# Performance work log

Measured on AMD Instinct MI355X. Metric: run time of the kernel, lower is better.

The kernel has to match this reference:

```python
import jax, jax.numpy as jnp
import numpy as np

B, S, E = 2, 2048, 2048
NH, NKV = 32, 8
HD = E // NH  # 64


def apply_rope(x, cos, sin):
    # x: [B, S, H, D]; cos/sin: [S, D]
    s, d = x.shape[1], x.shape[3]
    c = cos[:s, :d][None, :, None, :]
    sn = sin[:s, :d][None, :, None, :]
    x_rot = jnp.concatenate([-x[..., d // 2:], x[..., : d // 2]], axis=-1)
    return x * c + x_rot * sn


def setup_inputs() -> dict:
    key = jax.random.key(0)
    ks = jax.random.split(key, 6)
    x = jax.random.normal(ks[0], (B, S, E), dtype=jnp.float32)
    mask = jnp.ones((B, S), dtype=bool)
    # RoPE tables [S, HD]
    inv_freq = 1.0 / (10000.0 ** (jnp.arange(0, HD, 2, dtype=jnp.float32) / HD))
    freqs = jnp.arange(S, dtype=jnp.float32)[:, None] * inv_freq[None, :]
    emb = jnp.concatenate([freqs, freqs], axis=-1)  # [S, HD]
    cos = jnp.cos(emb)
    sin = jnp.sin(emb)
    sc = 1.0 / np.sqrt(E)
    Wq = jax.random.normal(ks[1], (E, E), dtype=jnp.float32) * sc
    Wk = jax.random.normal(ks[2], (NKV * HD, E), dtype=jnp.float32) * sc
    Wv = jax.random.normal(ks[3], (NKV * HD, E), dtype=jnp.float32) * sc
    Wo = jax.random.normal(ks[4], (E, E), dtype=jnp.float32) * sc
    return {"x": x, "mask": mask, "cos": cos, "sin": sin,
            "Wq": Wq, "Wk": Wk, "Wv": Wv, "Wo": Wo}


def reference(x, mask, cos, sin, Wq, Wk, Wv, Wo):
    b, s, e = x.shape
    scale = 1.0 / np.sqrt(HD)
    q = (x @ Wq.T).reshape(b, s, NH, HD)
    k = (x @ Wk.T).reshape(b, s, NKV, HD)
    v = (x @ Wv.T).reshape(b, s, NKV, HD)
    q = apply_rope(q, cos, sin)
    k = apply_rope(k, cos, sin)
    rep = NH // NKV
    # expand kv heads: [B,S,NKV,HD] -> [B,S,NH,HD]
    k = jnp.repeat(k, rep, axis=2)
    v = jnp.repeat(v, rep, axis=2)
    # [B,H,S,S]
    scores = jnp.einsum('bqhd,bkhd->bhqk', q, k) * scale
    causal = jnp.tril(jnp.ones((s, s), dtype=bool))
    combined = mask[:, None, None, :] & causal[None, None, :, :]
    scores = jnp.where(combined, scores, -jnp.inf)
    attn = jax.nn.softmax(scores, axis=-1)
    ctx = jnp.einsum('bhqk,bkhd->bqhd', attn, v).reshape(b, s, e)
    return ctx @ Wo.T
```

## Files before the change

### kernel.cpp

```cpp
#include <hip/hip_runtime.h>


typedef __attribute__((ext_vector_type(4))) float f32x4;
typedef __attribute__((ext_vector_type(16))) float f32x16;
typedef __attribute__((ext_vector_type(8))) __bf16 bf16x8;

#define SCL 0.18033688011112042f

__device__ __forceinline__ short f2bf(float f) {
  union { float f; unsigned u; } c; c.f = f;
  unsigned r = c.u + 0x7FFFu + ((c.u >> 16) & 1u);
  return (short)(r >> 16);
}

#define GLOAD16(g, l)                                                      \
  __builtin_amdgcn_global_load_lds(                                        \
      (const __attribute__((address_space(1))) unsigned int*)(g),          \
      (__attribute__((address_space(3))) unsigned int*)(l), 16, 0, 0)

#define VM_WAIT6() asm volatile("s_waitcnt vmcnt(6)" ::: "memory")
#define VM_WAIT4() asm volatile("s_waitcnt vmcnt(4)" ::: "memory")
#define VM_WAIT0() asm volatile("s_waitcnt vmcnt(0)" ::: "memory")
#define BARRIER()                        \
  do {                                   \
    __builtin_amdgcn_s_barrier();        \
    asm volatile("" ::: "memory");       \
  } while (0)

__device__ __forceinline__ f32x16 mfma32(bf16x8 a, bf16x8 b, f32x16 c) {
  return __builtin_amdgcn_mfma_f32_32x32x16_bf16(a, b, c, 0, 0, 0);
}

__global__ void conv_bf16(const float* __restrict__ src, short* __restrict__ dst, int n) {
  int i = (blockIdx.x * blockDim.x + threadIdx.x) * 4;
  if (i >= n) return;
  float4 v = *(const float4*)(src + i);
  *(short4*)(dst + i) = make_short4(f2bf(v.x), f2bf(v.y), f2bf(v.z), f2bf(v.w));
}

template <int EPI>
__global__ __launch_bounds__(512)
void gemm256(const short* __restrict__ A, const short* __restrict__ B,
             float* __restrict__ C, short* __restrict__ outQ,
             short* __restrict__ outK, short* __restrict__ outV,
             const float* __restrict__ cosT, const float* __restrict__ sinT,
             int M, int N, int K) {
  extern __shared__ short lds[];
  short* Asb = lds;
  short* Bsb = lds + 3 * 16384;
  const int tid = threadIdx.x;
  const int lane = tid & 63;
  const int wid = tid >> 6;
  const int wm = wid >> 1;
  const int wn = wid & 1;
  const int l5 = lane >> 5, lc5 = lane & 31;

  const int nwg = gridDim.x;
  const int cpx = nwg >> 3;
  const int swz = ((int)blockIdx.x & 7) * cpx + ((int)blockIdx.x >> 3);
  const int MT = M >> 8;
  const int mt = swz % MT, nt = swz / MT;
  const int m0 = mt << 8, n0 = nt << 7;

  const int srow = tid >> 3;
  const int gsl = (tid & 7) ^ (srow & 7);
  const short* Ag = A + (size_t)(m0 + srow) * K + gsl * 8;
  const short* Bg = B + (size_t)(n0 + srow) * K + gsl * 8;

  auto STAGE = [&](int k0, int buf) {
    short* ad = Asb + buf * 16384 + tid * 8;
    const short* ag = Ag + k0;
#pragma unroll
    for (int p = 0; p < 4; ++p)
      GLOAD16(ag + (size_t)(p * 64) * K, ad + p * 4096);
    short* bd = Bsb + buf * 8192 + tid * 8;
    const short* bg = Bg + k0;
#pragma unroll
    for (int p = 0; p < 2; ++p)
      GLOAD16(bg + (size_t)(p * 64) * K, bd + p * 4096);
  };

  f32x16 acc[2][2] = {};

  STAGE(0, 0);
  STAGE(64, 1);
  const int nk = K >> 6;
  for (int t = 0; t < nk; ++t) {
    if (t + 1 < nk) VM_WAIT6(); else VM_WAIT0();
    BARRIER();
    if (t + 2 < nk) STAGE((t + 2) << 6, (t + 2) % 3);
    const short* Ab = Asb + (t % 3) * 16384;
    const short* Bb = Bsb + (t % 3) * 8192;

    bf16x8 bfr[2][4];
#pragma unroll
    for (int ni = 0; ni < 2; ++ni) {
      const int row = (2 * wn + ni) * 32 + lc5;
#pragma unroll
      for (int s = 0; s < 4; ++s)
        bfr[ni][s] = *(const bf16x8*)(Bb + row * 64 + (((2 * s + l5) ^ (row & 7)) << 3));
    }
#pragma unroll
    for (int mi = 0; mi < 2; ++mi) {
      const int row = (2 * wm + mi) * 32 + lc5;
      bf16x8 af[4];
#pragma unroll
      for (int s = 0; s < 4; ++s)
        af[s] = *(const bf16x8*)(Ab + row * 64 + (((2 * s + l5) ^ (row & 7)) << 3));
      __builtin_amdgcn_s_setprio(1);
#pragma unroll
      for (int s = 0; s < 4; ++s) {
        acc[mi][0] = mfma32(af[s], bfr[0][s], acc[mi][0]);
        acc[mi][1] = mfma32(af[s], bfr[1][s], acc[mi][1]);
      }
      __builtin_amdgcn_s_setprio(0);
    }
  }

  if constexpr (EPI == 0) {
#pragma unroll
    for (int mi = 0; mi < 2; ++mi) {
      const int rb = m0 + (2 * wm + mi) * 32 + 4 * l5;
#pragma unroll
      for (int ni = 0; ni < 2; ++ni) {
        const int c = n0 + (2 * wn + ni) * 32 + lc5;
#pragma unroll
        for (int r = 0; r < 16; ++r)
          C[(size_t)(rb + (r & 3) + 8 * (r >> 2)) * N + c] = acc[mi][ni][r];
      }
    }
  } else {
    const int c0 = n0 + wn * 64 + lc5;
#pragma unroll
    for (int mi = 0; mi < 2; ++mi) {
      const int rb = m0 + (2 * wm + mi) * 32 + 4 * l5;
#pragma unroll
      for (int r = 0; r < 16; ++r) {
        const int row = rb + (r & 3) + 8 * (r >> 2);
        const int s = row & 2047;
        const float x0 = acc[mi][0][r], x1 = acc[mi][1][r];
        if (c0 < 2048) {
          const float cs = cosT[s * 64 + lc5], sn = sinT[s * 64 + lc5];
          outQ[(size_t)row * 2048 + c0] = f2bf((x0 * cs - x1 * sn) * SCL);
          outQ[(size_t)row * 2048 + c0 + 32] = f2bf((x1 * cs + x0 * sn) * SCL);
        } else if (c0 < 2560) {
          const float cs = cosT[s * 64 + lc5], sn = sinT[s * 64 + lc5];
          outK[(size_t)row * 512 + (c0 - 2048)] = f2bf(x0 * cs - x1 * sn);
          outK[(size_t)row * 512 + (c0 - 2048) + 32] = f2bf(x1 * cs + x0 * sn);
        } else {
          outV[(size_t)row * 512 + (c0 - 2560)] = f2bf(x0);
          outV[(size_t)row * 512 + (c0 - 2560) + 32] = f2bf(x1);
        }
      }
    }
  }
}

__global__ void transpose_v(const short* __restrict__ vtmp, short* __restrict__ vt) {
  __shared__ short Ls[64 * 66];
  int s0 = blockIdx.x * 64;
  int h = blockIdx.y;
  int b = blockIdx.z;
  int tid = threadIdx.x;
#pragma unroll
  for (int it = 0; it < 16; ++it) {
    int lin = it * 256 + tid;
    int r = lin >> 6, c = lin & 63;
    Ls[c * 66 + r] = vtmp[(size_t)(b * 2048 + s0 + r) * 512 + h * 64 + c];
  }
  __syncthreads();
#pragma unroll
  for (int it = 0; it < 16; ++it) {
    int lin = it * 256 + tid;
    int d = lin >> 6, c2 = lin & 63;
    vt[((size_t)((b * 8 + h) * 64 + d)) * 2048 + s0 + c2] = Ls[d * 66 + c2];
  }
}

__global__ __launch_bounds__(256, 2)
void attn(const short* __restrict__ Q, const short* __restrict__ Kk,
          const short* __restrict__ Vt, short* __restrict__ O) {
  const int p = blockIdx.x;
  const int h = blockIdx.y;
  const int b = blockIdx.z;
  const int kvh = h >> 2;
  const int tid = threadIdx.x;
  const int lane = tid & 63;
  const int w = tid >> 6;
  const int l5 = lane >> 5;
  const int lc5 = lane & 31;

  __shared__ short Ks[3][4096];
  __shared__ short Vs[3][4096];

  const short* kbs = Kk + (size_t)b * 2048 * 512 + kvh * 64;
  const short* vbs = Vt + (size_t)((b * 8 + kvh) * 64) * 2048;

  const int srow = tid >> 3;
  const int sslot = tid & 7;
  const int gs = sslot ^ (srow & 7);

  auto STAGE = [&](int kt, int buf) {
    const short* kp = kbs + (size_t)(kt * 64 + srow) * 512 + gs * 8;
    GLOAD16(kp, &Ks[buf][tid * 8]);
    GLOAD16(kp + 32 * 512, &Ks[buf][tid * 8 + 2048]);
    const short* vp = vbs + (size_t)srow * 2048 + kt * 64 + gs * 8;
    GLOAD16(vp, &Vs[buf][tid * 8]);
    GLOAD16(vp + 32 * 2048, &Vs[buf][tid * 8 + 2048]);
  };

  const int rx = lc5 & 7;

#pragma unroll 1
  for (int pass = 0; pass < 2; ++pass) {
    const int qb = pass == 0 ? (15 - p) : p;
    const int q0 = qb * 128;
    const int qrow = q0 + w * 32 + lc5;
    const int ktmax = 2 * qb + 1;

    bf16x8 qreg[4];
    const short* qbase = Q + (size_t)(b * 2048 + qrow) * 2048 + h * 64 + l5 * 8;
#pragma unroll
    for (int s = 0; s < 4; ++s) qreg[s] = *(const bf16x8*)(qbase + s * 16);

    f32x16 oa0 = {}, oa1 = {};
    float mrow = -1e30f, lrow = 0.f;

    __syncthreads();
    STAGE(0, 0);
    STAGE(1, 1);

    for (int kt = 0; kt <= ktmax; ++kt) {
      if (kt < ktmax) VM_WAIT4(); else VM_WAIT0();
      BARRIER();
      if (kt + 2 <= ktmax) STAGE(kt + 2, (kt + 2) % 3);
      const int cur = kt % 3;

      if (kt * 64 <= q0 + w * 32 + 31) {
        f32x16 sa0 = {}, sa1 = {};
        __builtin_amdgcn_s_setprio(1);
#pragma unroll
        for (int s = 0; s < 4; ++s) {
          const int so = (((2 * s + l5) ^ rx) << 3);
          bf16x8 k0f = *(const bf16x8*)(&Ks[cur][lc5 * 64 + so]);
          bf16x8 k1f = *(const bf16x8*)(&Ks[cur][(32 + lc5) * 64 + so]);
          sa0 = mfma32(k0f, qreg[s], sa0);
          sa1 = mfma32(k1f, qreg[s], sa1);
        }
        __builtin_amdgcn_s_setprio(0);

        if (kt * 64 + 63 > q0 + w * 32) {
          const int kbase = kt * 64 + 4 * l5;
#pragma unroll
          for (int r = 0; r < 16; ++r) {
            int k = kbase + (r & 3) + 8 * (r >> 2);
            if (k > qrow) sa0[r] = -1e30f;
            if (k + 32 > qrow) sa1[r] = -1e30f;
          }
        }

        float mx = -1e30f;
#pragma unroll
        for (int r = 0; r < 16; ++r) mx = fmaxf(mx, fmaxf(sa0[r], sa1[r]));
        mx = fmaxf(mx, __shfl_xor(mx, 32));
        if (!__all(mx <= mrow + 8.f)) {
          float nm = fmaxf(mrow, mx);
          float rs = exp2f(mrow - nm);
          mrow = nm;
          lrow *= rs;
#pragma unroll
          for (int r = 0; r < 16; ++r) { oa0[r] *= rs; oa1[r] *= rs; }
        }
        float ps = 0.f;
#pragma unroll
        for (int r = 0; r < 16; ++r) {
          float p0 = exp2f(sa0[r] - mrow);
          float p1 = exp2f(sa1[r] - mrow);
          sa0[r] = p0; sa1[r] = p1;
          ps += p0 + p1;
        }
        ps += __shfl_xor(ps, 32);
        lrow += ps;

        unsigned pk0[8], pk1[8];
#pragma unroll
        for (int a = 0; a < 8; ++a) {
          asm("v_cvt_pk_bf16_f32 %0, %1, %2" : "=v"(pk0[a]) : "v"(sa0[2 * a]), "v"(sa0[2 * a + 1]));
          asm("v_cvt_pk_bf16_f32 %0, %1, %2" : "=v"(pk1[a]) : "v"(sa1[2 * a]), "v"(sa1[2 * a + 1]));
        }

        __builtin_amdgcn_s_setprio(1);
#pragma unroll
        for (int s = 0; s < 4; ++s) {
          const int c = s & 1;
          unsigned x0 = (s < 2) ? pk0[4 * c + 0] : pk1[4 * c + 0];
          unsigned y0 = (s < 2) ? pk0[4 * c + 2] : pk1[4 * c + 2];
          unsigned x1 = (s < 2) ? pk0[4 * c + 1] : pk1[4 * c + 1];
          unsigned y1 = (s < 2) ? pk0[4 * c + 3] : pk1[4 * c + 3];
          asm("v_permlane32_swap_b32 %0, %1" : "+v"(x0), "+v"(y0));
          asm("v_permlane32_swap_b32 %0, %1" : "+v"(x1), "+v"(y1));
          union { unsigned u[4]; bf16x8 v; } pf;
          pf.u[0] = x0; pf.u[1] = x1; pf.u[2] = y0; pf.u[3] = y1;
          const int so = (((2 * s + l5) ^ rx) << 3);
          bf16x8 v0 = *(const bf16x8*)(&Vs[cur][lc5 * 64 + so]);
          bf16x8 v1 = *(const bf16x8*)(&Vs[cur][(32 + lc5) * 64 + so]);
          oa0 = mfma32(v0, pf.v, oa0);
          oa1 = mfma32(v1, pf.v, oa1);
        }
        __builtin_amdgcn_s_setprio(0);
      }
    }

    float inv = 1.0f / lrow;
    short* ob = O + (size_t)(b * 2048 + qrow) * 2048 + h * 64 + 4 * l5;
#pragma unroll
    for (int g = 0; g < 4; ++g) {
      *(short4*)(ob + 8 * g) =
          make_short4(f2bf(oa0[4 * g + 0] * inv), f2bf(oa0[4 * g + 1] * inv),
                      f2bf(oa0[4 * g + 2] * inv), f2bf(oa0[4 * g + 3] * inv));
      *(short4*)(ob + 32 + 8 * g) =
          make_short4(f2bf(oa1[4 * g + 0] * inv), f2bf(oa1[4 * g + 1] * inv),
                      f2bf(oa1[4 * g + 2] * inv), f2bf(oa1[4 * g + 3] * inv));
    }
  }
}

extern "C" void kernel_launch(void* const* d_in, const int* in_sizes, int n_in,
                              void* d_out, int out_size, void* d_ws, size_t ws_size,
                              hipStream_t stream) {
  (void)in_sizes; (void)n_in; (void)out_size; (void)ws_size;
  const float* x    = (const float*)d_in[0];
  const float* cosT = (const float*)d_in[2];
  const float* sinT = (const float*)d_in[3];
  const float* Wq   = (const float*)d_in[4];
  const float* Wk   = (const float*)d_in[5];
  const float* Wv   = (const float*)d_in[6];
  const float* Wo   = (const float*)d_in[7];

  char* ws = (char*)d_ws;
  short* xb   = (short*)(ws + 0);
  short* Wqob = (short*)(ws + 16777216);
  short* Wkvb = (short*)(ws + 25165824);
  short* qr   = (short*)(ws + 29360128);
  short* kb   = (short*)(ws + 46137344);
  short* vtmp = (short*)(ws + 50331648);
  short* vt   = (short*)(ws + 54525952);
  short* ctx  = (short*)(ws + 58720256);

  const int LDSB = 3 * (16384 + 8192) * 2;
  {
    auto* f0 = gemm256<0>;
    auto* f1 = gemm256<1>;
    hipFuncSetAttribute((const void*)f0, hipFuncAttributeMaxDynamicSharedMemorySize, LDSB);
    hipFuncSetAttribute((const void*)f1, hipFuncAttributeMaxDynamicSharedMemorySize, LDSB);
  }

  conv_bf16<<<8192, 256, 0, stream>>>(x, xb, 8388608);
  conv_bf16<<<4096, 256, 0, stream>>>(Wq, Wqob, 4194304);
  conv_bf16<<<1024, 256, 0, stream>>>(Wk, Wkvb, 1048576);
  conv_bf16<<<1024, 256, 0, stream>>>(Wv, Wkvb + 1048576, 1048576);

  gemm256<1><<<16 * 24, 512, LDSB, stream>>>(xb, Wqob, nullptr, qr, kb, vtmp,
                                             cosT, sinT, 4096, 3072, 2048);

  transpose_v<<<dim3(32, 8, 2), 256, 0, stream>>>(vtmp, vt);
  conv_bf16<<<4096, 256, 0, stream>>>(Wo, Wqob, 4194304);

  attn<<<dim3(8, 32, 2), 256, 0, stream>>>(qr, kb, vt, ctx);

  gemm256<0><<<16 * 16, 512, LDSB, stream>>>(ctx, Wqob, (float*)d_out, nullptr,
                                             nullptr, nullptr, nullptr, nullptr,
                                             4096, 2048, 2048);
}
```

Before: 349.6 us.

## Split GEMM K-tile across wave groups with LDS reduction; tree-reduce softmax max and sum

The 256x128 GEMM now assigns each wave a 128x64 output tile. The two wave groups each take half of every 64-wide K slice, so fewer LDS fragment loads are issued per MFMA. The partial accumulators are summed through LDS in the epilogue, which adds barriers and LDS traffic plus doubles accumulator registers. The attention softmax also replaces serial max and sum chains with tree reductions to shorten dependency latency.

```diff
diff --git a/kernel.cpp b/kernel.cpp
--- a/kernel.cpp
+++ b/kernel.cpp
@@ -51,8 +51,9 @@
   const int tid = threadIdx.x;
   const int lane = tid & 63;
   const int wid = tid >> 6;
-  const int wm = wid >> 1;
-  const int wn = wid & 1;
+  const int wm = wid & 1;
+  const int wn = (wid >> 1) & 1;
+  const int kg = wid >> 2;
   const int l5 = lane >> 5, lc5 = lane & 31;
 
   const int nwg = gridDim.x;
@@ -80,7 +81,7 @@
       GLOAD16(bg + (size_t)(p * 64) * K, bd + p * 4096);
   };
 
-  f32x16 acc[2][2] = {};
+  f32x16 acc[4][2] = {};
 
   STAGE(0, 0);
   STAGE(64, 1);
@@ -92,64 +93,80 @@
     const short* Ab = Asb + (t % 3) * 16384;
     const short* Bb = Bsb + (t % 3) * 8192;
 
-    bf16x8 bfr[2][4];
-#pragma unroll
-    for (int ni = 0; ni < 2; ++ni) {
-      const int row = (2 * wn + ni) * 32 + lc5;
-#pragma unroll
-      for (int s = 0; s < 4; ++s)
-        bfr[ni][s] = *(const bf16x8*)(Bb + row * 64 + (((2 * s + l5) ^ (row & 7)) << 3));
-    }
-#pragma unroll
-    for (int mi = 0; mi < 2; ++mi) {
-      const int row = (2 * wm + mi) * 32 + lc5;
-      bf16x8 af[4];
-#pragma unroll
-      for (int s = 0; s < 4; ++s)
-        af[s] = *(const bf16x8*)(Ab + row * 64 + (((2 * s + l5) ^ (row & 7)) << 3));
-      __builtin_amdgcn_s_setprio(1);
-#pragma unroll
-      for (int s = 0; s < 4; ++s) {
-        acc[mi][0] = mfma32(af[s], bfr[0][s], acc[mi][0]);
-        acc[mi][1] = mfma32(af[s], bfr[1][s], acc[mi][1]);
-      }
-      __builtin_amdgcn_s_setprio(0);
-    }
-  }
-
-  if constexpr (EPI == 0) {
-#pragma unroll
-    for (int mi = 0; mi < 2; ++mi) {
-      const int rb = m0 + (2 * wm + mi) * 32 + 4 * l5;
+    bf16x8 af[4][2], bfv[2][2];
+#pragma unroll
+    for (int si = 0; si < 2; ++si) {
+      const int ch = 2 * (2 * kg + si) + l5;
+#pragma unroll
+      for (int mi = 0; mi < 4; ++mi) {
+        const int row = wm * 128 + mi * 32 + lc5;
+        af[mi][si] = *(const bf16x8*)(Ab + row * 64 + ((ch ^ (row & 7)) << 3));
+      }
 #pragma unroll
       for (int ni = 0; ni < 2; ++ni) {
-        const int c = n0 + (2 * wn + ni) * 32 + lc5;
+        const int row = wn * 64 + ni * 32 + lc5;
+        bfv[ni][si] = *(const bf16x8*)(Bb + row * 64 + ((ch ^ (row & 7)) << 3));
+      }
+    }
+    __builtin_amdgcn_s_setprio(1);
+#pragma unroll
+    for (int mi = 0; mi < 4; ++mi)
+#pragma unroll
+      for (int ni = 0; ni < 2; ++ni)
+#pragma unroll
+        for (int si = 0; si < 2; ++si)
+          acc[mi][ni] = mfma32(af[mi][si], bfv[ni][si], acc[mi][ni]);
+    __builtin_amdgcn_s_setprio(0);
+  }
+
+  float* red = (float*)(lds + 32768);
+  const int slab = (wm * 2 + wn) * 2048;
+#pragma unroll
+  for (int mi = 0; mi < 4; ++mi) {
+    __syncthreads();
+    if (kg == 1) {
+#pragma unroll
+      for (int ni = 0; ni < 2; ++ni)
 #pragma unroll
         for (int r = 0; r < 16; ++r)
-          C[(size_t)(rb + (r & 3) + 8 * (r >> 2)) * N + c] = acc[mi][ni][r];
-      }
-    }
-  } else {
-    const int c0 = n0 + wn * 64 + lc5;
-#pragma unroll
-    for (int mi = 0; mi < 2; ++mi) {
-      const int rb = m0 + (2 * wm + mi) * 32 + 4 * l5;
+          red[slab + (ni * 16 + r) * 64 + lane] = acc[mi][ni][r];
+    }
+    __syncthreads();
+    if (kg == 0) {
+      f32x16 a0 = acc[mi][0], a1 = acc[mi][1];
 #pragma unroll
       for (int r = 0; r < 16; ++r) {
-        const int row = rb + (r & 3) + 8 * (r >> 2);
-        const int s = row & 2047;
-        const float x0 = acc[mi][0][r], x1 = acc[mi][1][r];
-        if (c0 < 2048) {
-          const float cs = cosT[s * 64 + lc5], sn = sinT[s * 64 + lc5];
-          outQ[(size_t)row * 2048 + c0] = f2bf((x0 * cs - x1 * sn) * SCL);
-          outQ[(size_t)row * 2048 + c0 + 32] = f2bf((x1 * cs + x0 * sn) * SCL);
-        } else if (c0 < 2560) {
-          const float cs = cosT[s * 64 + lc5], sn = sinT[s * 64 + lc5];
-          outK[(size_t)row * 512 + (c0 - 2048)] = f2bf(x0 * cs - x1 * sn);
-          outK[(size_t)row * 512 + (c0 - 2048) + 32] = f2bf(x1 * cs + x0 * sn);
-        } else {
-          outV[(size_t)row * 512 + (c0 - 2560)] = f2bf(x0);
-          outV[(size_t)row * 512 + (c0 - 2560) + 32] = f2bf(x1);
+        a0[r] += red[slab + r * 64 + lane];
+        a1[r] += red[slab + (16 + r) * 64 + lane];
+      }
+      const int rb = m0 + wm * 128 + mi * 32 + 4 * l5;
+      if constexpr (EPI == 0) {
+        const int cb = n0 + wn * 64 + lc5;
+#pragma unroll
+        for (int r = 0; r < 16; ++r) {
+          const int row = rb + (r & 3) + 8 * (r >> 2);
+          C[(size_t)row * N + cb] = a0[r];
+          C[(size_t)row * N + cb + 32] = a1[r];
+        }
+      } else {
+        const int c0 = n0 + wn * 64 + lc5;
+#pragma unroll
+        for (int r = 0; r < 16; ++r) {
+          const int row = rb + (r & 3) + 8 * (r >> 2);
+          const int s = row & 2047;
+          const float x0 = a0[r], x1 = a1[r];
+          if (c0 < 2048) {
+            const float cs = cosT[s * 64 + lc5], sn = sinT[s * 64 + lc5];
+            outQ[(size_t)row * 2048 + c0] = f2bf((x0 * cs - x1 * sn) * SCL);
+            outQ[(size_t)row * 2048 + c0 + 32] = f2bf((x1 * cs + x0 * sn) * SCL);
+          } else if (c0 < 2560) {
+            const float cs = cosT[s * 64 + lc5], sn = sinT[s * 64 + lc5];
+            outK[(size_t)row * 512 + (c0 - 2048)] = f2bf(x0 * cs - x1 * sn);
+            outK[(size_t)row * 512 + (c0 - 2048) + 32] = f2bf(x1 * cs + x0 * sn);
+          } else {
+            outV[(size_t)row * 512 + (c0 - 2560)] = f2bf(x0);
+            outV[(size_t)row * 512 + (c0 - 2560) + 32] = f2bf(x1);
+          }
         }
       }
     }
@@ -259,9 +276,13 @@
           }
         }
 
-        float mx = -1e30f;
-#pragma unroll
-        for (int r = 0; r < 16; ++r) mx = fmaxf(mx, fmaxf(sa0[r], sa1[r]));
+        float tm[8];
+#pragma unroll
+        for (int r = 0; r < 8; ++r)
+          tm[r] = fmaxf(fmaxf(sa0[r], sa0[r + 8]), fmaxf(sa1[r], sa1[r + 8]));
+#pragma unroll
+        for (int r = 0; r < 4; ++r) tm[r] = fmaxf(tm[r], tm[r + 4]);
+        float mx = fmaxf(fmaxf(tm[0], tm[2]), fmaxf(tm[1], tm[3]));
         mx = fmaxf(mx, __shfl_xor(mx, 32));
         if (!__all(mx <= mrow + 8.f)) {
           float nm = fmaxf(mrow, mx);
@@ -271,14 +292,18 @@
 #pragma unroll
           for (int r = 0; r < 16; ++r) { oa0[r] *= rs; oa1[r] *= rs; }
         }
-        float ps = 0.f;
 #pragma unroll
         for (int r = 0; r < 16; ++r) {
-          float p0 = exp2f(sa0[r] - mrow);
-          float p1 = exp2f(sa1[r] - mrow);
-          sa0[r] = p0; sa1[r] = p1;
-          ps += p0 + p1;
-        }
+          sa0[r] = exp2f(sa0[r] - mrow);
+          sa1[r] = exp2f(sa1[r] - mrow);
+        }
+        float ts[8];
+#pragma unroll
+        for (int r = 0; r < 8; ++r)
+          ts[r] = (sa0[r] + sa0[r + 8]) + (sa1[r] + sa1[r + 8]);
+#pragma unroll
+        for (int r = 0; r < 4; ++r) ts[r] += ts[r + 4];
+        float ps = (ts[0] + ts[2]) + (ts[1] + ts[3]);
         ps += __shfl_xor(ps, 32);
         lrow += ps;
 
```

Result: slower. 366.4 us (+4.8%).
